# Optimization experiments

Measured on AMD Instinct MI355X. Metric: run time of the kernel, lower is better.

The kernel has to match this reference:

```python
import jax, jax.numpy as jnp
import numpy as np

B = 16384          # batch_size (z_i rows)
D = 2048           # latent_size
PRIOR = 0.3
PRIOR_PRIME = 0.5
GAMMA = 1.0
BETA = 0.0


def setup_inputs() -> dict:
    key = jax.random.key(0)
    k1, k2, k3, k4 = jax.random.split(key, 4)
    z_i = jax.random.normal(k1, (B, D), dtype=jnp.float32)
    z_j = jax.random.normal(k2, (B, D), dtype=jnp.float32)
    # nn.Linear(latent_size, 1): weight (1, D) stored flat as (D,), bias scalar
    W = jax.random.normal(k3, (D,), dtype=jnp.float32) / np.sqrt(D)
    b = jax.random.normal(k4, (), dtype=jnp.float32) * 0.01
    return {"z_i": z_i, "z_j": z_j, "W": W, "b": b}


def reference(z_i, z_j, W, b):
    # pred = flatten(Linear(cat(z_i, z_j)))  -> (2B,)
    z = jnp.concatenate([z_i, z_j], axis=0)
    pred = z @ W + b                        # (n,) with n = 2B
    n = pred.shape[0]
    batch = n // 2
    # targets matrix: -1 everywhere, +1 on diagonal and at the (i, i+B)/(i+B, i)
    # contrastive pairs -> each row i has exactly 2 positives: i and pair(i).
    idx = jnp.arange(batch)
    pair = jnp.concatenate([idx + batch, idx])   # pair(i) for every row i
    s_pos = jax.nn.sigmoid(pred)    # loss_func(-x) = sigmoid(x)
    s_neg = jax.nn.sigmoid(-pred)   # loss_func(x)  = sigmoid(-x)
    # per-row sums of the onnpu_loss (row i of targets used as target vector)
    sum_y_pos = s_neg + s_neg[pair]                 # sum(loss(pos*inp)*pos)
    sum_y_pos_inv = s_pos + s_pos[pair]             # sum(loss(-pos*inp)*pos)
    total_s_pos = jnp.sum(s_pos)
    sum_y_unl = total_s_pos - s_pos - s_pos[pair]   # sum(loss(-unl*inp)*unl)
    n_positive = jnp.maximum(1.0, 2.0)              # max(min_count, 2)
    n_unlabeled = jnp.maximum(1.0, jnp.float32(n) - 2.0)
    positive_risk = PRIOR_PRIME / n_positive * sum_y_pos
    negative_risk = ((1.0 - PRIOR_PRIME) / (n_unlabeled * (1.0 - PRIOR)) * sum_y_unl
                     - (1.0 - PRIOR_PRIME) * PRIOR / (n_positive * (1.0 - PRIOR)) * sum_y_pos_inv)
    # nnPU branch: if negative_risk < -beta -> -gamma * negative_risk
    loss_rows = jnp.where(negative_risk < -BETA,
                          -GAMMA * negative_risk,
                          positive_risk + negative_risk)
    return jnp.mean(loss_rows)
```

## Files before the change

kernel.cpp:

```cpp
#include <hip/hip_runtime.h>
#include <math.h>

#define B_ROWS 16384
#define DLAT   2048
#define NTOT   (2 * B_ROWS)
#define NBLK1  (NTOT / 8)
#define NBLK3  128

__global__ __launch_bounds__(256, 4) void k_dot_sig(
    const float* __restrict__ zi, const float* __restrict__ zj,
    const float* __restrict__ W,  const float* __restrict__ bptr,
    float* __restrict__ sp, float* __restrict__ partial)
{
    const int lane = threadIdx.x & 63;
    const int wv   = threadIdx.x >> 6;
    const int r0   = (blockIdx.x * 4 + wv) * 2;
    const int r1   = r0 + 1;

    const float4* pa = (const float4*)((r0 < B_ROWS)
        ? zi + (size_t)r0 * DLAT : zj + (size_t)(r0 - B_ROWS) * DLAT);
    const float4* pb = (const float4*)((r1 < B_ROWS)
        ? zi + (size_t)r1 * DLAT : zj + (size_t)(r1 - B_ROWS) * DLAT);

    float4 za[8], zb[8];
    #pragma unroll
    for (int i = 0; i < 8; ++i) za[i] = pa[i * 64 + lane];
    #pragma unroll
    for (int i = 0; i < 8; ++i) zb[i] = pb[i * 64 + lane];

    const float4* w4 = (const float4*)W;
    float aA = 0.0f, aB = 0.0f;
    #pragma unroll
    for (int i = 0; i < 8; ++i) {
        float4 w = w4[i * 64 + lane];
        aA += za[i].x * w.x + za[i].y * w.y + za[i].z * w.z + za[i].w * w.w;
        aB += zb[i].x * w.x + zb[i].y * w.y + zb[i].z * w.z + zb[i].w * w.w;
    }

    #pragma unroll
    for (int off = 32; off > 0; off >>= 1) {
        aA += __shfl_xor(aA, off, 64);
        aB += __shfl_xor(aB, off, 64);
    }

    __shared__ float s8[8];
    if (lane == 0) {
        float b  = bptr[0];
        float sA = 1.0f / (1.0f + expf(-(aA + b)));
        float sB = 1.0f / (1.0f + expf(-(aB + b)));
        sp[r0] = sA; sp[r1] = sB;
        s8[wv * 2] = sA; s8[wv * 2 + 1] = sB;
    }
    __syncthreads();
    if (threadIdx.x == 0)
        partial[blockIdx.x] = ((s8[0] + s8[1]) + (s8[2] + s8[3]))
                            + ((s8[4] + s8[5]) + (s8[6] + s8[7]));
}

__global__ __launch_bounds__(1024) void k_total(
    const float* __restrict__ partial, float* __restrict__ total)
{
    __shared__ float red[1024];
    const int t = threadIdx.x;
    float s = 0.0f;
    for (int i = t; i < NBLK1; i += 1024) s += partial[i];
    red[t] = s;
    __syncthreads();
    #pragma unroll
    for (int st = 512; st > 0; st >>= 1) {
        if (t < st) red[t] += red[t + st];
        __syncthreads();
    }
    if (t == 0) total[0] = red[0];
}

__global__ __launch_bounds__(256) void k_loss(
    const float* __restrict__ sp, const float* __restrict__ total,
    float* __restrict__ lp)
{
    const int t = threadIdx.x;
    const int r = blockIdx.x * 256 + t;

    const float tot = total[0];
    const float c1  = 0.5f / (((float)NTOT - 2.0f) * 0.7f);
    const float c2  = (0.5f * 0.3f) / (2.0f * 0.7f);

    float S2  = sp[r] + sp[r ^ B_ROWS];
    float pos = 0.25f * (2.0f - S2);
    float neg = c1 * (tot - S2) - c2 * S2;
    float l   = (neg < 0.0f) ? -neg : (pos + neg);

    __shared__ float red[256];
    red[t] = l;
    __syncthreads();
    #pragma unroll
    for (int st = 128; st > 0; st >>= 1) {
        if (t < st) red[t] += red[t + st];
        __syncthreads();
    }
    if (t == 0) lp[blockIdx.x] = red[0];
}

__global__ __launch_bounds__(128) void k_mean(
    const float* __restrict__ lp, float* __restrict__ out)
{
    __shared__ float red[128];
    const int t = threadIdx.x;
    red[t] = lp[t];
    __syncthreads();
    #pragma unroll
    for (int st = 64; st > 0; st >>= 1) {
        if (t < st) red[t] += red[t + st];
        __syncthreads();
    }
    if (t == 0) out[0] = red[0] / (float)NTOT;
}

extern "C" void kernel_launch(void* const* d_in, const int* in_sizes, int n_in,
                              void* d_out, int out_size, void* d_ws, size_t ws_size,
                              hipStream_t stream) {
    const float* zi = (const float*)d_in[0];
    const float* zj = (const float*)d_in[1];
    const float* W  = (const float*)d_in[2];
    const float* b  = (const float*)d_in[3];

    float* sp      = (float*)d_ws;
    float* partial = sp + NTOT;
    float* lp      = partial + NBLK1;
    float* total   = lp + NBLK3;
    float* out     = (float*)d_out;

    k_dot_sig<<<NBLK1, 256, 0, stream>>>(zi, zj, W, b, sp, partial);
    k_total <<<1, 1024, 0, stream>>>(partial, total);
    k_loss  <<<NBLK3, 256, 0, stream>>>(sp, total, lp);
    k_mean  <<<1, 128, 0, stream>>>(lp, out);
}
```

Measured before the change: 280.3 us.

## Use persistent blocks with double-buffered global-to-LDS async row streaming

Replaces the one-block-per-8-rows GEMV with 512 persistent blocks. Each block keeps W in registers and streams 4-row tiles into double-buffered LDS through global_load_lds, with manual vmcnt waits and barriers. This aims to overlap the next tile's loads with the current tile's dot products and to avoid reloading W in every block. The cost is fewer resident waves and in-flight loads per CU than the old many-block design, plus two barriers per tile.

```diff
diff --git a/kernel.cpp b/kernel.cpp
--- a/kernel.cpp
+++ b/kernel.cpp
@@ -4,71 +4,103 @@
 #define B_ROWS 16384
 #define DLAT   2048
 #define NTOT   (2 * B_ROWS)
-#define NBLK1  (NTOT / 8)
+#define TILE_ROWS 4
+#define TILE_FLOATS (TILE_ROWS * DLAT)
+#define NTILES (NTOT / TILE_ROWS)
+#define NBLK1  512
+#define TILES_PER_BLK (NTILES / NBLK1)
 #define NBLK3  128
 
-__global__ __launch_bounds__(256, 4) void k_dot_sig(
+typedef __attribute__((address_space(3))) unsigned char lds_t;
+typedef const __attribute__((address_space(1))) unsigned char glb_t;
+
+__device__ __forceinline__ void gld_lds16(const float* g, float* l) {
+    __builtin_amdgcn_global_load_lds((glb_t*)(const void*)g,
+                                     (lds_t*)(void*)l, 16, 0, 0);
+}
+
+__global__ __launch_bounds__(256) void k_dot_sig(
     const float* __restrict__ zi, const float* __restrict__ zj,
     const float* __restrict__ W,  const float* __restrict__ bptr,
     float* __restrict__ sp, float* __restrict__ partial)
 {
+    __shared__ float buf[2][TILE_FLOATS];
+    __shared__ float wsum[4];
+
     const int lane = threadIdx.x & 63;
     const int wv   = threadIdx.x >> 6;
-    const int r0   = (blockIdx.x * 4 + wv) * 2;
-    const int r1   = r0 + 1;
 
-    const float4* pa = (const float4*)((r0 < B_ROWS)
-        ? zi + (size_t)r0 * DLAT : zj + (size_t)(r0 - B_ROWS) * DLAT);
-    const float4* pb = (const float4*)((r1 < B_ROWS)
-        ? zi + (size_t)r1 * DLAT : zj + (size_t)(r1 - B_ROWS) * DLAT);
+    const float4* w4p = (const float4*)W;
+    float4 w[8];
+    #pragma unroll
+    for (int i = 0; i < 8; ++i) w[i] = w4p[i * 64 + lane];
+    const float bias = bptr[0];
 
-    float4 za[8], zb[8];
-    #pragma unroll
-    for (int i = 0; i < 8; ++i) za[i] = pa[i * 64 + lane];
-    #pragma unroll
-    for (int i = 0; i < 8; ++i) zb[i] = pb[i * 64 + lane];
+    const int t0 = blockIdx.x * TILES_PER_BLK;
 
-    const float4* w4 = (const float4*)W;
-    float aA = 0.0f, aB = 0.0f;
-    #pragma unroll
-    for (int i = 0; i < 8; ++i) {
-        float4 w = w4[i * 64 + lane];
-        aA += za[i].x * w.x + za[i].y * w.y + za[i].z * w.z + za[i].w * w.w;
-        aB += zb[i].x * w.x + zb[i].y * w.y + zb[i].z * w.z + zb[i].w * w.w;
+    auto stage = [&](int bi, int tile) {
+        const int r = tile * TILE_ROWS;
+        const float* gb = (r < B_ROWS) ? zi + (size_t)r * DLAT
+                                       : zj + (size_t)(r - B_ROWS) * DLAT;
+        const float* g = gb + wv * 2048 + lane * 4;
+        float* l = &buf[bi][wv * 2048];
+        #pragma unroll
+        for (int i = 0; i < 8; ++i)
+            gld_lds16(g + i * 256, l + i * 256);
+    };
+
+    stage(0, t0);
+
+    float bsum = 0.0f;
+
+    for (int t = 0; t < TILES_PER_BLK; ++t) {
+        const int cur = t & 1;
+        if (t + 1 < TILES_PER_BLK) {
+            stage(cur ^ 1, t0 + t + 1);
+            asm volatile("s_waitcnt vmcnt(8)" ::: "memory");
+        } else {
+            asm volatile("s_waitcnt vmcnt(0)" ::: "memory");
+        }
+        __builtin_amdgcn_s_barrier();
+        asm volatile("" ::: "memory");
+
+        const float4* rowp = (const float4*)&buf[cur][wv * 2048];
+        float acc = 0.0f;
+        #pragma unroll
+        for (int i = 0; i < 8; ++i) {
+            float4 z = rowp[i * 64 + lane];
+            acc += z.x * w[i].x + z.y * w[i].y + z.z * w[i].z + z.w * w[i].w;
+        }
+        #pragma unroll
+        for (int off = 32; off > 0; off >>= 1)
+            acc += __shfl_xor(acc, off, 64);
+
+        if (lane == 0) {
+            int row = (t0 + t) * TILE_ROWS + wv;
+            float s = 1.0f / (1.0f + expf(-(acc + bias)));
+            sp[row] = s;
+            bsum += s;
+        }
+        asm volatile("" ::: "memory");
+        __builtin_amdgcn_s_barrier();
     }
 
-    #pragma unroll
-    for (int off = 32; off > 0; off >>= 1) {
-        aA += __shfl_xor(aA, off, 64);
-        aB += __shfl_xor(aB, off, 64);
-    }
-
-    __shared__ float s8[8];
-    if (lane == 0) {
-        float b  = bptr[0];
-        float sA = 1.0f / (1.0f + expf(-(aA + b)));
-        float sB = 1.0f / (1.0f + expf(-(aB + b)));
-        sp[r0] = sA; sp[r1] = sB;
-        s8[wv * 2] = sA; s8[wv * 2 + 1] = sB;
-    }
+    if (lane == 0) wsum[wv] = bsum;
     __syncthreads();
     if (threadIdx.x == 0)
-        partial[blockIdx.x] = ((s8[0] + s8[1]) + (s8[2] + s8[3]))
-                            + ((s8[4] + s8[5]) + (s8[6] + s8[7]));
+        partial[blockIdx.x] = (wsum[0] + wsum[1]) + (wsum[2] + wsum[3]);
 }
 
-__global__ __launch_bounds__(1024) void k_total(
+__global__ __launch_bounds__(512) void k_total(
     const float* __restrict__ partial, float* __restrict__ total)
 {
-    __shared__ float red[1024];
+    __shared__ float red[512];
     const int t = threadIdx.x;
-    float s = 0.0f;
-    for (int i = t; i < NBLK1; i += 1024) s += partial[i];
-    red[t] = s;
+    red[t] = partial[t];
     __syncthreads();
     #pragma unroll
-    for (int st = 512; st > 0; st >>= 1) {
-        if (t < st) red[t] += red[t + st];
+    for (int s = 256; s > 0; s >>= 1) {
+        if (t < s) red[t] += red[t + s];
         __syncthreads();
     }
     if (t == 0) total[0] = red[0];
@@ -94,8 +126,8 @@
     red[t] = l;
     __syncthreads();
     #pragma unroll
-    for (int st = 128; st > 0; st >>= 1) {
-        if (t < st) red[t] += red[t + st];
+    for (int s = 128; s > 0; s >>= 1) {
+        if (t < s) red[t] += red[t + s];
         __syncthreads();
     }
     if (t == 0) lp[blockIdx.x] = red[0];
@@ -109,8 +141,8 @@
     red[t] = lp[t];
     __syncthreads();
     #pragma unroll
-    for (int st = 64; st > 0; st >>= 1) {
-        if (t < st) red[t] += red[t + st];
+    for (int s = 64; s > 0; s >>= 1) {
+        if (t < s) red[t] += red[t + s];
         __syncthreads();
     }
     if (t == 0) out[0] = red[0] / (float)NTOT;
@@ -131,7 +163,7 @@
     float* out     = (float*)d_out;
 
     k_dot_sig<<<NBLK1, 256, 0, stream>>>(zi, zj, W, b, sp, partial);
-    k_total <<<1, 1024, 0, stream>>>(partial, total);
+    k_total <<<1, 512, 0, stream>>>(partial, total);
     k_loss  <<<NBLK3, 256, 0, stream>>>(sp, total, lp);
     k_mean  <<<1, 128, 0, stream>>>(lp, out);
 }
```

Measured after the change: 289.4 us. +3.3%, slower.

## Split dot-sigmoid kernel per input half, stream z_i with nontemporal loads

Applied to the files above, without the earlier changes.

Replaces the single dot-product kernel with two launches of a templated kernel, one for z_i and one for z_j, which removes the per-row pointer selection. The z_i launch uses nontemporal loads so that z_i is less likely to evict z_j from the last-level cache, letting the second launch read z_j from cache if it is still resident from an earlier call. Loads are now issued inside the FMA loop rather than all up front, and the min-blocks launch bound is dropped. The cost is an extra kernel launch and possibly less memory-level parallelism per wave.

```diff
diff --git a/kernel.cpp b/kernel.cpp
--- a/kernel.cpp
+++ b/kernel.cpp
@@ -4,37 +4,41 @@
 #define B_ROWS 16384
 #define DLAT   2048
 #define NTOT   (2 * B_ROWS)
-#define NBLK1  (NTOT / 8)
+#define NBLK_H 2048
+#define NPART  (2 * NBLK_H)
 #define NBLK3  128
 
-__global__ __launch_bounds__(256, 4) void k_dot_sig(
-    const float* __restrict__ zi, const float* __restrict__ zj,
-    const float* __restrict__ W,  const float* __restrict__ bptr,
-    float* __restrict__ sp, float* __restrict__ partial)
+typedef float nfloat4 __attribute__((ext_vector_type(4)));
+
+template<bool NT>
+__global__ __launch_bounds__(256) void k_half(
+    const float* __restrict__ z, const float* __restrict__ W,
+    const float* __restrict__ bptr, float* __restrict__ sp,
+    float* __restrict__ partial)
 {
     const int lane = threadIdx.x & 63;
     const int wv   = threadIdx.x >> 6;
     const int r0   = (blockIdx.x * 4 + wv) * 2;
     const int r1   = r0 + 1;
 
-    const float4* pa = (const float4*)((r0 < B_ROWS)
-        ? zi + (size_t)r0 * DLAT : zj + (size_t)(r0 - B_ROWS) * DLAT);
-    const float4* pb = (const float4*)((r1 < B_ROWS)
-        ? zi + (size_t)r1 * DLAT : zj + (size_t)(r1 - B_ROWS) * DLAT);
+    const nfloat4* pa = (const nfloat4*)(z + (size_t)r0 * DLAT);
+    const nfloat4* pb = (const nfloat4*)(z + (size_t)r1 * DLAT);
+    const nfloat4* w4 = (const nfloat4*)W;
 
-    float4 za[8], zb[8];
-    #pragma unroll
-    for (int i = 0; i < 8; ++i) za[i] = pa[i * 64 + lane];
-    #pragma unroll
-    for (int i = 0; i < 8; ++i) zb[i] = pb[i * 64 + lane];
-
-    const float4* w4 = (const float4*)W;
     float aA = 0.0f, aB = 0.0f;
     #pragma unroll
     for (int i = 0; i < 8; ++i) {
-        float4 w = w4[i * 64 + lane];
-        aA += za[i].x * w.x + za[i].y * w.y + za[i].z * w.z + za[i].w * w.w;
-        aB += zb[i].x * w.x + zb[i].y * w.y + zb[i].z * w.z + zb[i].w * w.w;
+        nfloat4 za, zb;
+        if constexpr (NT) {
+            za = __builtin_nontemporal_load(&pa[i * 64 + lane]);
+            zb = __builtin_nontemporal_load(&pb[i * 64 + lane]);
+        } else {
+            za = pa[i * 64 + lane];
+            zb = pb[i * 64 + lane];
+        }
+        nfloat4 w = w4[i * 64 + lane];
+        aA += za.x * w.x + za.y * w.y + za.z * w.z + za.w * w.w;
+        aB += zb.x * w.x + zb.y * w.y + zb.z * w.z + zb.w * w.w;
     }
 
     #pragma unroll
@@ -63,7 +67,7 @@
     __shared__ float red[1024];
     const int t = threadIdx.x;
     float s = 0.0f;
-    for (int i = t; i < NBLK1; i += 1024) s += partial[i];
+    for (int i = t; i < NPART; i += 1024) s += partial[i];
     red[t] = s;
     __syncthreads();
     #pragma unroll
@@ -126,12 +130,13 @@
 
     float* sp      = (float*)d_ws;
     float* partial = sp + NTOT;
-    float* lp      = partial + NBLK1;
+    float* lp      = partial + NPART;
     float* total   = lp + NBLK3;
     float* out     = (float*)d_out;
 
-    k_dot_sig<<<NBLK1, 256, 0, stream>>>(zi, zj, W, b, sp, partial);
-    k_total <<<1, 1024, 0, stream>>>(partial, total);
-    k_loss  <<<NBLK3, 256, 0, stream>>>(sp, total, lp);
-    k_mean  <<<1, 128, 0, stream>>>(lp, out);
+    k_half<true ><<<NBLK_H, 256, 0, stream>>>(zi, W, b, sp,          partial);
+    k_half<false><<<NBLK_H, 256, 0, stream>>>(zj, W, b, sp + B_ROWS, partial + NBLK_H);
+    k_total<<<1, 1024, 0, stream>>>(partial, total);
+    k_loss <<<NBLK3, 256, 0, stream>>>(sp, total, lp);
+    k_mean <<<1, 128, 0, stream>>>(lp, out);
 }
```

Result: faster. 272.2 us (-2.9%).
